# Kernel tuning notes

Hardware: AMD Instinct MI355X
Metric: run time of the kernel (lower is better)

The kernel has to match this reference:

```python
import jax, jax.numpy as jnp
import numpy as np
from jax import lax

B, N, C = 8, 8192, 64
NPOINT, NSAMPLE, RADIUS = 2048, 32, 0.2
EPS = 1e-5


def setup_inputs() -> dict:
    key = jax.random.key(0)
    ks = jax.random.split(key, 14)
    xyz = jax.random.uniform(ks[0], (B, 3, N), dtype=jnp.float32)
    points = jax.random.normal(ks[1], (B, C, N), dtype=jnp.float32)
    dims = [(67, 64), (64, 64), (64, 128)]
    inp = {"xyz": xyz, "points": points}
    for i, (cin, cout) in enumerate(dims, start=1):
        inp[f"W{i}"] = jax.random.normal(ks[2 * i], (cout, cin), dtype=jnp.float32) / np.sqrt(cin)
        inp[f"b{i}"] = jnp.zeros((cout,), jnp.float32)
        inp[f"g{i}"] = jnp.ones((cout,), jnp.float32)
        inp[f"be{i}"] = jnp.zeros((cout,), jnp.float32)
    return inp


def farthest_point_sample(x, npoint):
    # x: [B, N, 3] -> [B, npoint] int32 indices
    b, n, _ = x.shape
    barange = jnp.arange(b)

    def step(carry, _):
        dist, far = carry
        centroid = x[barange, far]                      # [B, 3]
        d = jnp.sum((x - centroid[:, None, :]) ** 2, -1)  # [B, N]
        dist = jnp.minimum(dist, d)
        return (dist, jnp.argmax(dist, -1)), far

    init = (jnp.full((b, n), 1e10, x.dtype), jnp.zeros((b,), jnp.int32))
    _, cents = lax.scan(step, init, None, length=npoint)
    return cents.T  # [B, npoint]


def square_distance(src, dst):
    # src: [B, S, 3], dst: [B, D, 3] -> [B, S, D]
    d = -2.0 * jnp.einsum('bsc,bdc->bsd', src, dst)
    d += jnp.sum(src ** 2, -1)[:, :, None]
    d += jnp.sum(dst ** 2, -1)[:, None, :]
    return d


def query_ball_point(radius, nsample, x, new_x):
    b, n, _ = x.shape
    sqr = square_distance(new_x, x)                    # [B, NP, N]
    idx = jnp.where(sqr > radius ** 2, n, jnp.arange(n)[None, None, :])
    idx = jnp.sort(idx, axis=-1)[:, :, :nsample]       # [B, NP, NS]
    first = idx[:, :, :1]
    return jnp.where(idx == n, first, idx)


def _bn_relu(x, g, be):
    # x: [B, NP, NS, Cout]; batchnorm over (B, NP, NS) per channel (training stats)
    m = x.mean((0, 1, 2))
    v = x.var((0, 1, 2))
    return jax.nn.relu((x - m) * lax.rsqrt(v + EPS) * g + be)


def reference(xyz, points, W1, b1, g1, be1, W2, b2, g2, be2, W3, b3, g3, be3):
    x = xyz.transpose(0, 2, 1)       # [B, N, 3]
    p = points.transpose(0, 2, 1)    # [B, N, C]
    bidx = jnp.arange(B)[:, None, None]

    fps_idx = farthest_point_sample(x, NPOINT)               # [B, NP]
    new_xyz = jnp.take_along_axis(x, fps_idx[:, :, None], 1)  # [B, NP, 3]
    idx = query_ball_point(RADIUS, NSAMPLE, x, new_xyz)       # [B, NP, NS]

    grouped_xyz = x[bidx, idx]                                # [B, NP, NS, 3]
    grouped_norm = grouped_xyz - new_xyz[:, :, None, :]
    grouped_p = p[bidx, idx]                                  # [B, NP, NS, C]
    feat = jnp.concatenate([grouped_norm, grouped_p], -1)     # [B, NP, NS, 3+C]

    for W, b, g, be in ((W1, b1, g1, be1), (W2, b2, g2, be2), (W3, b3, g3, be3)):
        feat = _bn_relu(jnp.einsum('bpsc,oc->bpso', feat, W) + b, g, be)

    new_points = jnp.max(feat, axis=2)                        # [B, NP, Cout]
    return new_xyz.transpose(0, 2, 1), new_points.transpose(0, 2, 1)
```

## Files before the change

### kernel.cpp

```cpp
#include <hip/hip_runtime.h>
#include <hip/hip_bf16.h>
#include <stdint.h>

#define NB 8
#define NPTS 8192
#define NCH 64
#define NPOINT 2048
#define NSAMPLE 32
#define R2 0.04f

#define DPP_MAX_STEP(C) { \
  int lo2_ = __builtin_amdgcn_update_dpp(0, (int)(unsigned int)key, (C), 0xf, 0xf, true); \
  int hi2_ = __builtin_amdgcn_update_dpp(0, (int)(unsigned int)(key>>32), (C), 0xf, 0xf, true); \
  unsigned long long k2_ = ((unsigned long long)(unsigned int)hi2_ << 32) | (unsigned int)lo2_; \
  if (k2_ > key) key = k2_; }

__global__ __launch_bounds__(512) void fps_kernel(const float* __restrict__ xyz,
                                                  float* __restrict__ out)
{
  const int t = threadIdx.x;
  const int wv = t >> 6, lane = t & 63;
  const int b = blockIdx.x;
  const float* xb = xyz + (size_t)b*3*NPTS;
  __shared__ float s_px[NPTS], s_py[NPTS], s_pz[NPTS];
  __shared__ float s_ox[NPOINT], s_oy[NPOINT], s_oz[NPOINT];
  __shared__ unsigned long long s_key[2][8];
  for (int e=t; e<NPTS; e+=512){
    s_px[e]=xb[e]; s_py[e]=xb[NPTS+e]; s_pz[e]=xb[2*NPTS+e];
  }
  float px[16], py[16], pz[16], dist[16];
  const int base = (wv<<10) + lane;
  #pragma unroll
  for (int k=0;k<16;k++){
    int i = base + (k<<6);
    px[k]=xb[i]; py[k]=xb[NPTS+i]; pz[k]=xb[2*NPTS+i];
    dist[k]=1e10f;
  }
  __syncthreads();
  float cx = s_px[0], cy = s_py[0], cz = s_pz[0];
  for (int s=0;s<NPOINT;s++){
    if (t==0){ s_ox[s]=cx; s_oy[s]=cy; s_oz[s]=cz; }
    float best = -1.0f; int bidx = 0;
    #pragma unroll
    for (int k=0;k<16;k++){
      float dx=__fsub_rn(px[k],cx), dy=__fsub_rn(py[k],cy), dz=__fsub_rn(pz[k],cz);
      float d = __fadd_rn(__fadd_rn(__fmul_rn(dx,dx),__fmul_rn(dy,dy)),__fmul_rn(dz,dz));
      float nd = d < dist[k] ? d : dist[k];
      dist[k]=nd;
      if (nd > best){ best = nd; bidx = base + (k<<6); }
    }
    unsigned long long key = ((unsigned long long)__float_as_uint(best) << 13)
                           | (unsigned long long)(8191 - bidx);
    DPP_MAX_STEP(0x111)
    DPP_MAX_STEP(0x112)
    DPP_MAX_STEP(0x114)
    DPP_MAX_STEP(0x118)
    DPP_MAX_STEP(0x142)
    DPP_MAX_STEP(0x143)
    if (lane==63) s_key[s&1][wv] = key;
    __syncthreads();
    const unsigned long long* kr = s_key[s&1];
    unsigned long long k0=kr[0],k1=kr[1],k2=kr[2],k3=kr[3],
                       k4=kr[4],k5=kr[5],k6=kr[6],k7=kr[7];
    unsigned long long m01=k0>k1?k0:k1, m23=k2>k3?k2:k3;
    unsigned long long m45=k4>k5?k4:k5, m67=k6>k7?k6:k7;
    unsigned long long m03=m01>m23?m01:m23, m47=m45>m67?m45:m67;
    unsigned long long mk = m03>m47?m03:m47;
    const int far = 8191 - (int)(mk & 8191ull);
    cx = s_px[far]; cy = s_py[far]; cz = s_pz[far];
  }
  __syncthreads();
  float* oxb = out + (size_t)b*3*NPOINT;
  for (int e=t; e<NPOINT; e+=512){
    oxb[e]          = s_ox[e];
    oxb[NPOINT+e]   = s_oy[e];
    oxb[2*NPOINT+e] = s_oz[e];
  }
}

__global__ __launch_bounds__(256) void ball_kernel(const float* __restrict__ xyz,
                                                   const float* __restrict__ nxyz,
                                                   int* __restrict__ ball_idx)
{
  __shared__ int s_buf[4][NSAMPLE];
  const int wv = threadIdx.x >> 6, lane = threadIdx.x & 63;
  const int g = blockIdx.x*4 + wv;
  const int b = g >> 11;
  const int s = g & 2047;
  const float* ob = nxyz + (size_t)b*3*NPOINT;
  const float cx = ob[s], cy = ob[NPOINT+s], cz = ob[2*NPOINT+s];
  const float csum = __fadd_rn(__fadd_rn(__fmul_rn(cx,cx),__fmul_rn(cy,cy)),__fmul_rn(cz,cz));
  const float* xb = xyz + (size_t)b*3*NPTS;
  int cnt = 0;
  for (int c0=0; c0<NPTS; c0+=64){
    const int i = c0 + lane;
    float x=xb[i], y=xb[NPTS+i], z=xb[2*NPTS+i];
    float dot  = __fmaf_rn(cz, z, __fmaf_rn(cy, y, __fmul_rn(cx, x)));
    float dsum = __fadd_rn(__fadd_rn(__fmul_rn(x,x),__fmul_rn(y,y)),__fmul_rn(z,z));
    float sqr  = __fadd_rn(__fadd_rn(__fmul_rn(-2.0f,dot), csum), dsum);
    bool in = (sqr <= R2);
    unsigned long long m = __ballot(in);
    int rank = cnt + __popcll(m & ((1ull<<lane)-1ull));
    if (in && rank < NSAMPLE) s_buf[wv][rank] = i;
    cnt += (int)__popcll(m);
    if (cnt >= NSAMPLE) break;
  }
  const int first = s_buf[wv][0];
  if (lane < NSAMPLE){
    int v = (lane < cnt) ? s_buf[wv][lane] : first;
    ball_idx[(size_t)g*NSAMPLE + lane] = v;
  }
}

__global__ __launch_bounds__(128) void mlp1_kernel(
    const float* __restrict__ xyz, const float* __restrict__ points,
    const float* __restrict__ nxyz, const int* __restrict__ ball_idx,
    const float* __restrict__ W1, const float* __restrict__ b1,
    float* __restrict__ z, float* __restrict__ part)
{
  __shared__ float wl[67*64];
  __shared__ float spA[128], spQ[128];
  const int t = threadIdx.x;
  const int m = blockIdx.x*128 + t;
  const int g = m >> 5;
  const int b = g >> 11;
  const int s = g & 2047;
  for (int e=t; e<67*64; e+=128){
    int o = e/67, c = e - o*67;
    wl[c*64+o] = W1[e];
  }
  const int idx = ball_idx[m];
  const float* xb = xyz + (size_t)b*3*NPTS;
  const float* ob = nxyz + (size_t)b*3*NPOINT;
  float f[67];
  f[0] = __fsub_rn(xb[idx],        ob[s]);
  f[1] = __fsub_rn(xb[NPTS+idx],   ob[NPOINT+s]);
  f[2] = __fsub_rn(xb[2*NPTS+idx], ob[2*NPOINT+s]);
  const float* pb = points + (size_t)b*NCH*NPTS;
  #pragma unroll
  for (int c=0;c<64;c++) f[3+c] = pb[(size_t)c*NPTS + idx];
  __syncthreads();
  float acc[64];
  #pragma unroll
  for (int o=0;o<64;o++) acc[o]=0.0f;
  #pragma unroll
  for (int c=0;c<67;c++){
    const float fc = f[c];
    const float* wr = &wl[c*64];
    #pragma unroll
    for (int q=0;q<16;q++){
      float4 w = *(const float4*)(wr + q*4);
      acc[q*4+0] = __fmaf_rn(fc, w.x, acc[q*4+0]);
      acc[q*4+1] = __fmaf_rn(fc, w.y, acc[q*4+1]);
      acc[q*4+2] = __fmaf_rn(fc, w.z, acc[q*4+2]);
      acc[q*4+3] = __fmaf_rn(fc, w.w, acc[q*4+3]);
    }
  }
  #pragma unroll
  for (int o=0;o<64;o++) acc[o] = __fadd_rn(acc[o], b1[o]);
  float* zr = z + (size_t)m*64;
  #pragma unroll
  for (int q=0;q<16;q++){
    float4 v; v.x=acc[q*4]; v.y=acc[q*4+1]; v.z=acc[q*4+2]; v.w=acc[q*4+3];
    *(float4*)(zr + q*4) = v;
  }
  float sA=0.f, sQ=0.f;
  const int oc = t & 63;
  for (int p=0;p<2;p++){
    __syncthreads();
    if ((t>>6)==p){
      const int r = t & 63;
      #pragma unroll
      for (int j=0;j<64;j++) wl[r*65+j] = acc[j];
    }
    __syncthreads();
    const int r0 = (t>>6)*32;
    for (int r=r0; r<r0+32; r++){
      float v = wl[r*65+oc];
      sA += v; sQ = __fmaf_rn(v,v,sQ);
    }
  }
  spA[t]=sA; spQ[t]=sQ;
  __syncthreads();
  if (t<64){
    part[(size_t)blockIdx.x*128 + t]      = spA[t]+spA[t+64];
    part[(size_t)blockIdx.x*128 + 64 + t] = spQ[t]+spQ[t+64];
  }
}

__global__ __launch_bounds__(128) void mlp2_kernel(
    float* __restrict__ z, const float* __restrict__ ab1,
    const float* __restrict__ W2, const float* __restrict__ b2,
    float* __restrict__ part)
{
  __shared__ float wl[67*64];
  __shared__ float spA[128], spQ[128];
  __shared__ float s_ab[128];
  const int t = threadIdx.x;
  const int m = blockIdx.x*128 + t;
  for (int e=t; e<64*64; e+=128){
    int o = e>>6, c = e&63;
    wl[c*64+o] = W2[e];
  }
  if (t<128) s_ab[t] = ab1[t];
  __syncthreads();
  float* zr = z + (size_t)m*64;
  float f[64];
  #pragma unroll
  for (int q=0;q<16;q++){
    float4 v = *(const float4*)(zr + q*4);
    float a0 = __fmaf_rn(v.x, s_ab[q*4+0], s_ab[64+q*4+0]);
    float a1 = __fmaf_rn(v.y, s_ab[q*4+1], s_ab[64+q*4+1]);
    float a2 = __fmaf_rn(v.z, s_ab[q*4+2], s_ab[64+q*4+2]);
    float a3 = __fmaf_rn(v.w, s_ab[q*4+3], s_ab[64+q*4+3]);
    f[q*4+0] = a0 > 0.f ? a0 : 0.f;
    f[q*4+1] = a1 > 0.f ? a1 : 0.f;
    f[q*4+2] = a2 > 0.f ? a2 : 0.f;
    f[q*4+3] = a3 > 0.f ? a3 : 0.f;
  }
  float acc[64];
  #pragma unroll
  for (int o=0;o<64;o++) acc[o]=0.0f;
  #pragma unroll
  for (int c=0;c<64;c++){
    const float fc = f[c];
    const float* wr = &wl[c*64];
    #pragma unroll
    for (int q=0;q<16;q++){
      float4 w = *(const float4*)(wr + q*4);
      acc[q*4+0] = __fmaf_rn(fc, w.x, acc[q*4+0]);
      acc[q*4+1] = __fmaf_rn(fc, w.y, acc[q*4+1]);
      acc[q*4+2] = __fmaf_rn(fc, w.z, acc[q*4+2]);
      acc[q*4+3] = __fmaf_rn(fc, w.w, acc[q*4+3]);
    }
  }
  #pragma unroll
  for (int o=0;o<64;o++) acc[o] = __fadd_rn(acc[o], b2[o]);
  #pragma unroll
  for (int q=0;q<16;q++){
    float4 v; v.x=acc[q*4]; v.y=acc[q*4+1]; v.z=acc[q*4+2]; v.w=acc[q*4+3];
    *(float4*)(zr + q*4) = v;
  }
  float sA=0.f, sQ=0.f;
  const int oc = t & 63;
  for (int p=0;p<2;p++){
    __syncthreads();
    if ((t>>6)==p){
      const int r = t & 63;
      #pragma unroll
      for (int j=0;j<64;j++) wl[r*65+j] = acc[j];
    }
    __syncthreads();
    const int r0 = (t>>6)*32;
    for (int r=r0; r<r0+32; r++){
      float v = wl[r*65+oc];
      sA += v; sQ = __fmaf_rn(v,v,sQ);
    }
  }
  spA[t]=sA; spQ[t]=sQ;
  __syncthreads();
  if (t<64){
    part[(size_t)blockIdx.x*128 + t]      = spA[t]+spA[t+64];
    part[(size_t)blockIdx.x*128 + 64 + t] = spQ[t]+spQ[t+64];
  }
}

__global__ __launch_bounds__(256) void mlp3_kernel(
    const float* __restrict__ z, const float* __restrict__ ab2,
    const float* __restrict__ W3, const float* __restrict__ b3,
    float* __restrict__ gmax, float* __restrict__ part)
{
  __shared__ float wl[128*65];
  __shared__ float spA[256], spQ[256];
  __shared__ float s_ab[128];
  const int t = threadIdx.x;
  const int m0 = blockIdx.x*128;
  const int sm = t>>1, h = t&1;
  const int m = m0 + sm;
  for (int e=t; e<64*128; e+=256){
    int o = e>>6, c = e&63;
    wl[c*128+o] = W3[e];
  }
  if (t<128) s_ab[t] = ab2[t];
  __syncthreads();
  const float* zr = z + (size_t)m*64;
  float f[64];
  #pragma unroll
  for (int q=0;q<16;q++){
    float4 v = *(const float4*)(zr + q*4);
    float a0 = __fmaf_rn(v.x, s_ab[q*4+0], s_ab[64+q*4+0]);
    float a1 = __fmaf_rn(v.y, s_ab[q*4+1], s_ab[64+q*4+1]);
    float a2 = __fmaf_rn(v.z, s_ab[q*4+2], s_ab[64+q*4+2]);
    float a3 = __fmaf_rn(v.w, s_ab[q*4+3], s_ab[64+q*4+3]);
    f[q*4+0] = a0 > 0.f ? a0 : 0.f;
    f[q*4+1] = a1 > 0.f ? a1 : 0.f;
    f[q*4+2] = a2 > 0.f ? a2 : 0.f;
    f[q*4+3] = a3 > 0.f ? a3 : 0.f;
  }
  float acc[64];
  #pragma unroll
  for (int o=0;o<64;o++) acc[o]=0.0f;
  #pragma unroll
  for (int c=0;c<64;c++){
    const float fc = f[c];
    const float* wr = &wl[c*128 + h*64];
    #pragma unroll
    for (int q=0;q<16;q++){
      float4 w = *(const float4*)(wr + q*4);
      acc[q*4+0] = __fmaf_rn(fc, w.x, acc[q*4+0]);
      acc[q*4+1] = __fmaf_rn(fc, w.y, acc[q*4+1]);
      acc[q*4+2] = __fmaf_rn(fc, w.z, acc[q*4+2]);
      acc[q*4+3] = __fmaf_rn(fc, w.w, acc[q*4+3]);
    }
  }
  #pragma unroll
  for (int j=0;j<64;j++) acc[j] = __fadd_rn(acc[j], b3[h*64+j]);
  for (int p=0;p<2;p++){
    __syncthreads();
    if (h==p){
      const int r = sm;
      #pragma unroll
      for (int j=0;j<64;j++) wl[r*65+j] = acc[j];
    }
    __syncthreads();
    const int oc = t & 63;
    const int q4 = t >> 6;
    float sA=0.f, sQ=0.f;
    for (int r=q4*32; r<q4*32+32; r++){
      float v = wl[r*65+oc];
      sA += v; sQ = __fmaf_rn(v,v,sQ);
    }
    spA[t]=sA; spQ[t]=sQ;
    __syncthreads();
    if (t<64){
      float A = spA[t]+spA[t+64]+spA[t+128]+spA[t+192];
      float Q = spQ[t]+spQ[t+64]+spQ[t+128]+spQ[t+192];
      part[(size_t)blockIdx.x*256 + p*64 + t]       = A;
      part[(size_t)blockIdx.x*256 + 128 + p*64 + t] = Q;
    }
  }
  #pragma unroll
  for (int off=2; off<64; off<<=1){
    #pragma unroll
    for (int j=0;j<64;j++){
      float ov = __shfl_xor(acc[j], off, 64);
      acc[j] = acc[j] > ov ? acc[j] : ov;
    }
  }
  const int lane = t & 63, w = t >> 6;
  const int gg = (m0>>5) + w;
  if (lane < 2){
    float* gp = gmax + (size_t)gg*128 + lane*64;
    #pragma unroll
    for (int q=0;q<16;q++){
      float4 v; v.x=acc[q*4]; v.y=acc[q*4+1]; v.z=acc[q*4+2]; v.w=acc[q*4+3];
      *(float4*)(gp + q*4) = v;
    }
  }
}

__global__ __launch_bounds__(64) void reduce_kernel(const float* __restrict__ part,
    const float* __restrict__ gw, const float* __restrict__ bew,
    float* __restrict__ ab, int cout, int nblk)
{
  const int o = blockIdx.x, t = threadIdx.x;
  const int stride = 2*cout;
  float A=0.f, Q=0.f;
  for (int i=t;i<nblk;i+=64){
    A += part[(size_t)i*stride + o];
    Q += part[(size_t)i*stride + cout + o];
  }
  #pragma unroll
  for (int off=1; off<64; off<<=1){
    A += __shfl_xor(A, off, 64);
    Q += __shfl_xor(Q, off, 64);
  }
  if (t==0){
    const float inv = 1.0f/524288.0f;
    float mean = A*inv;
    float var  = Q*inv - mean*mean;
    float a = gw[o] / sqrtf(var + 1e-5f);
    ab[o] = a;
    ab[cout+o] = bew[o] - mean*a;
  }
}

__global__ __launch_bounds__(256) void final_kernel(const float* __restrict__ gmax,
    const float* __restrict__ ab3, float* __restrict__ out)
{
  __shared__ float tile[32*129];
  __shared__ float s_a[128], s_b[128];
  const int t = threadIdx.x;
  const int b = blockIdx.x >> 6;
  const int s0 = (blockIdx.x & 63)*32;
  if (t<128){ s_a[t]=ab3[t]; s_b[t]=ab3[128+t]; }
  const float* gp = gmax + ((size_t)b*NPOINT + s0)*128;
  for (int e=t; e<32*32; e+=256){
    int r = e>>5, q = e&31;
    float4 v = *(const float4*)(gp + r*128 + q*4);
    tile[r*129 + q*4+0]=v.x; tile[r*129 + q*4+1]=v.y;
    tile[r*129 + q*4+2]=v.z; tile[r*129 + q*4+3]=v.w;
  }
  __syncthreads();
  float* ob = out + 49152 + (size_t)b*128*NPOINT;
  for (int e=t; e<128*32; e+=256){
    int o = e>>5, ls = e&31;
    float v = tile[ls*129 + o];
    v = __fmaf_rn(v, s_a[o], s_b[o]);
    v = v > 0.f ? v : 0.f;
    ob[(size_t)o*NPOINT + s0 + ls] = v;
  }
}

extern "C" void kernel_launch(void* const* d_in, const int* in_sizes, int n_in,
                              void* d_out, int out_size, void* d_ws, size_t ws_size,
                              hipStream_t stream)
{
  const float* xyz    = (const float*)d_in[0];
  const float* points = (const float*)d_in[1];
  const float* W1 = (const float*)d_in[2];
  const float* b1 = (const float*)d_in[3];
  const float* g1 = (const float*)d_in[4];
  const float* be1= (const float*)d_in[5];
  const float* W2 = (const float*)d_in[6];
  const float* b2 = (const float*)d_in[7];
  const float* g2 = (const float*)d_in[8];
  const float* be2= (const float*)d_in[9];
  const float* W3 = (const float*)d_in[10];
  const float* b3 = (const float*)d_in[11];
  const float* g3 = (const float*)d_in[12];
  const float* be3= (const float*)d_in[13];
  float* out = (float*)d_out;
  char* ws = (char*)d_ws;
  float* z     = (float*)(ws);
  float* gmax  = (float*)(ws + 134217728);
  int*   ball  = (int*)  (ws + 142606336);
  float* part1 = (float*)(ws + 144703488);
  float* part2 = (float*)(ws + 146800640);
  float* part3 = (float*)(ws + 148897792);
  float* ab1   = (float*)(ws + 153092096);
  float* ab2   = (float*)(ws + 153092608);
  float* ab3   = (float*)(ws + 153093120);

  hipLaunchKernelGGL(fps_kernel,   dim3(NB),   dim3(512),  0, stream, xyz, out);
  hipLaunchKernelGGL(ball_kernel,  dim3(4096), dim3(256),  0, stream, xyz, out, ball);
  hipLaunchKernelGGL(mlp1_kernel,  dim3(4096), dim3(128),  0, stream, xyz, points, out, ball, W1, b1, z, part1);
  hipLaunchKernelGGL(reduce_kernel,dim3(64),   dim3(64),   0, stream, part1, g1, be1, ab1, 64, 4096);
  hipLaunchKernelGGL(mlp2_kernel,  dim3(4096), dim3(128),  0, stream, z, ab1, W2, b2, part2);
  hipLaunchKernelGGL(reduce_kernel,dim3(64),   dim3(64),   0, stream, part2, g2, be2, ab2, 64, 4096);
  hipLaunchKernelGGL(mlp3_kernel,  dim3(4096), dim3(256),  0, stream, z, ab2, W3, b3, gmax, part3);
  hipLaunchKernelGGL(reduce_kernel,dim3(128),  dim3(64),   0, stream, part3, g3, be3, ab3, 128, 4096);
  hipLaunchKernelGGL(final_kernel, dim3(512),  dim3(256),  0, stream, gmax, ab3, out);
}
```

Baseline: 2.683 ms.

## Fuse ball query into MLP1, pre-transpose points, store activations channel-major

Adds a transpose kernel so each gathered neighbour's 64 features form one contiguous row read with float4 loads, replacing 64 strided scalar gathers. The ball query is merged into the first MLP kernel, which removes the ball_idx round trip through global memory and one launch. The intermediate z buffer becomes channel-major per block, so per-thread accesses in mlp1/2/3 coalesce across threads. The cost is an extra transpose pass over the point features and a ball-query stage that now uses only two waves per block, run serially for four centroids.

```diff
diff --git a/kernel.cpp b/kernel.cpp
--- a/kernel.cpp
+++ b/kernel.cpp
@@ -78,68 +78,89 @@
   }
 }
 
-__global__ __launch_bounds__(256) void ball_kernel(const float* __restrict__ xyz,
-                                                   const float* __restrict__ nxyz,
-                                                   int* __restrict__ ball_idx)
-{
-  __shared__ int s_buf[4][NSAMPLE];
-  const int wv = threadIdx.x >> 6, lane = threadIdx.x & 63;
-  const int g = blockIdx.x*4 + wv;
-  const int b = g >> 11;
-  const int s = g & 2047;
-  const float* ob = nxyz + (size_t)b*3*NPOINT;
-  const float cx = ob[s], cy = ob[NPOINT+s], cz = ob[2*NPOINT+s];
-  const float csum = __fadd_rn(__fadd_rn(__fmul_rn(cx,cx),__fmul_rn(cy,cy)),__fmul_rn(cz,cz));
-  const float* xb = xyz + (size_t)b*3*NPTS;
-  int cnt = 0;
-  for (int c0=0; c0<NPTS; c0+=64){
-    const int i = c0 + lane;
-    float x=xb[i], y=xb[NPTS+i], z=xb[2*NPTS+i];
-    float dot  = __fmaf_rn(cz, z, __fmaf_rn(cy, y, __fmul_rn(cx, x)));
-    float dsum = __fadd_rn(__fadd_rn(__fmul_rn(x,x),__fmul_rn(y,y)),__fmul_rn(z,z));
-    float sqr  = __fadd_rn(__fadd_rn(__fmul_rn(-2.0f,dot), csum), dsum);
-    bool in = (sqr <= R2);
-    unsigned long long m = __ballot(in);
-    int rank = cnt + __popcll(m & ((1ull<<lane)-1ull));
-    if (in && rank < NSAMPLE) s_buf[wv][rank] = i;
-    cnt += (int)__popcll(m);
-    if (cnt >= NSAMPLE) break;
-  }
-  const int first = s_buf[wv][0];
-  if (lane < NSAMPLE){
-    int v = (lane < cnt) ? s_buf[wv][lane] : first;
-    ball_idx[(size_t)g*NSAMPLE + lane] = v;
-  }
-}
-
-__global__ __launch_bounds__(128) void mlp1_kernel(
-    const float* __restrict__ xyz, const float* __restrict__ points,
-    const float* __restrict__ nxyz, const int* __restrict__ ball_idx,
+__global__ __launch_bounds__(256) void transpose_kernel(const float* __restrict__ points,
+                                                        float* __restrict__ pt)
+{
+  __shared__ float tile[64][65];
+  const int t = threadIdx.x;
+  const int b  = blockIdx.x >> 7;
+  const int n0 = (blockIdx.x & 127) << 6;
+  const int tx = t & 63, ty = t >> 6;
+  #pragma unroll
+  for (int r=0; r<16; r++){
+    const int c = ty*16 + r;
+    tile[c][tx] = points[(size_t)b*NCH*NPTS + (size_t)c*NPTS + n0 + tx];
+  }
+  __syncthreads();
+  #pragma unroll
+  for (int r=0; r<16; r++){
+    const int n = ty*16 + r;
+    pt[((size_t)b*NPTS + n0 + n)*64 + tx] = tile[tx][n];
+  }
+}
+
+__global__ __launch_bounds__(128) void ballmlp1_kernel(
+    const float* __restrict__ xyz, const float* __restrict__ pt,
+    const float* __restrict__ nxyz,
     const float* __restrict__ W1, const float* __restrict__ b1,
     float* __restrict__ z, float* __restrict__ part)
 {
   __shared__ float wl[67*64];
   __shared__ float spA[128], spQ[128];
-  const int t = threadIdx.x;
-  const int m = blockIdx.x*128 + t;
-  const int g = m >> 5;
-  const int b = g >> 11;
-  const int s = g & 2047;
+  __shared__ int s_buf[4][NSAMPLE];
+  __shared__ int s_cnt[4];
+  __shared__ float s_ctr[4][3];
+  const int t = threadIdx.x;
+  const int blk = blockIdx.x;
   for (int e=t; e<67*64; e+=128){
     int o = e/67, c = e - o*67;
     wl[c*64+o] = W1[e];
   }
-  const int idx = ball_idx[m];
+  const int wv = t>>6, lane = t&63;
+  for (int sub=0; sub<2; sub++){
+    const int gi2 = wv*2 + sub;
+    const int g = blk*4 + gi2;
+    const int b = g >> 11;
+    const int s = g & 2047;
+    const float* ob = nxyz + (size_t)b*3*NPOINT;
+    const float cx = ob[s], cy = ob[NPOINT+s], cz = ob[2*NPOINT+s];
+    if (lane==0){ s_ctr[gi2][0]=cx; s_ctr[gi2][1]=cy; s_ctr[gi2][2]=cz; }
+    const float csum = __fadd_rn(__fadd_rn(__fmul_rn(cx,cx),__fmul_rn(cy,cy)),__fmul_rn(cz,cz));
+    const float* xb = xyz + (size_t)b*3*NPTS;
+    int cnt = 0;
+    for (int c0=0; c0<NPTS; c0+=64){
+      const int i = c0 + lane;
+      float x=xb[i], y=xb[NPTS+i], zz=xb[2*NPTS+i];
+      float dot  = __fmaf_rn(cz, zz, __fmaf_rn(cy, y, __fmul_rn(cx, x)));
+      float dsum = __fadd_rn(__fadd_rn(__fmul_rn(x,x),__fmul_rn(y,y)),__fmul_rn(zz,zz));
+      float sqr  = __fadd_rn(__fadd_rn(__fmul_rn(-2.0f,dot), csum), dsum);
+      bool in = (sqr <= R2);
+      unsigned long long mm = __ballot(in);
+      int rank = cnt + __popcll(mm & ((1ull<<lane)-1ull));
+      if (in && rank < NSAMPLE) s_buf[gi2][rank] = i;
+      cnt += (int)__popcll(mm);
+      if (cnt >= NSAMPLE) break;
+    }
+    if (lane==0) s_cnt[gi2] = cnt;
+  }
+  __syncthreads();
+  const int gi = t>>5, lane2 = t&31;
+  const int g = blk*4 + gi;
+  const int b = g >> 11;
+  const int cnt = s_cnt[gi];
+  const int first = s_buf[gi][0];
+  const int idx = (lane2 < cnt) ? s_buf[gi][lane2] : first;
   const float* xb = xyz + (size_t)b*3*NPTS;
-  const float* ob = nxyz + (size_t)b*3*NPOINT;
   float f[67];
-  f[0] = __fsub_rn(xb[idx],        ob[s]);
-  f[1] = __fsub_rn(xb[NPTS+idx],   ob[NPOINT+s]);
-  f[2] = __fsub_rn(xb[2*NPTS+idx], ob[2*NPOINT+s]);
-  const float* pb = points + (size_t)b*NCH*NPTS;
-  #pragma unroll
-  for (int c=0;c<64;c++) f[3+c] = pb[(size_t)c*NPTS + idx];
-  __syncthreads();
+  f[0] = __fsub_rn(xb[idx],        s_ctr[gi][0]);
+  f[1] = __fsub_rn(xb[NPTS+idx],   s_ctr[gi][1]);
+  f[2] = __fsub_rn(xb[2*NPTS+idx], s_ctr[gi][2]);
+  const float* pr = pt + ((size_t)b*NPTS + idx)*64;
+  #pragma unroll
+  for (int q=0;q<16;q++){
+    float4 v = *(const float4*)(pr + q*4);
+    f[3+q*4+0]=v.x; f[3+q*4+1]=v.y; f[3+q*4+2]=v.z; f[3+q*4+3]=v.w;
+  }
   float acc[64];
   #pragma unroll
   for (int o=0;o<64;o++) acc[o]=0.0f;
@@ -158,12 +179,9 @@
   }
   #pragma unroll
   for (int o=0;o<64;o++) acc[o] = __fadd_rn(acc[o], b1[o]);
-  float* zr = z + (size_t)m*64;
-  #pragma unroll
-  for (int q=0;q<16;q++){
-    float4 v; v.x=acc[q*4]; v.y=acc[q*4+1]; v.z=acc[q*4+2]; v.w=acc[q*4+3];
-    *(float4*)(zr + q*4) = v;
-  }
+  float* zb = z + (size_t)blk*8192;
+  #pragma unroll
+  for (int c=0;c<64;c++) zb[c*128 + t] = acc[c];
   float sA=0.f, sQ=0.f;
   const int oc = t & 63;
   for (int p=0;p<2;p++){
@@ -183,8 +201,8 @@
   spA[t]=sA; spQ[t]=sQ;
   __syncthreads();
   if (t<64){
-    part[(size_t)blockIdx.x*128 + t]      = spA[t]+spA[t+64];
-    part[(size_t)blockIdx.x*128 + 64 + t] = spQ[t]+spQ[t+64];
+    part[(size_t)blk*128 + t]      = spA[t]+spA[t+64];
+    part[(size_t)blk*128 + 64 + t] = spQ[t]+spQ[t+64];
   }
 }
 
@@ -197,26 +215,19 @@
   __shared__ float spA[128], spQ[128];
   __shared__ float s_ab[128];
   const int t = threadIdx.x;
-  const int m = blockIdx.x*128 + t;
   for (int e=t; e<64*64; e+=128){
     int o = e>>6, c = e&63;
     wl[c*64+o] = W2[e];
   }
   if (t<128) s_ab[t] = ab1[t];
   __syncthreads();
-  float* zr = z + (size_t)m*64;
+  float* zb = z + (size_t)blockIdx.x*8192;
   float f[64];
   #pragma unroll
-  for (int q=0;q<16;q++){
-    float4 v = *(const float4*)(zr + q*4);
-    float a0 = __fmaf_rn(v.x, s_ab[q*4+0], s_ab[64+q*4+0]);
-    float a1 = __fmaf_rn(v.y, s_ab[q*4+1], s_ab[64+q*4+1]);
-    float a2 = __fmaf_rn(v.z, s_ab[q*4+2], s_ab[64+q*4+2]);
-    float a3 = __fmaf_rn(v.w, s_ab[q*4+3], s_ab[64+q*4+3]);
-    f[q*4+0] = a0 > 0.f ? a0 : 0.f;
-    f[q*4+1] = a1 > 0.f ? a1 : 0.f;
-    f[q*4+2] = a2 > 0.f ? a2 : 0.f;
-    f[q*4+3] = a3 > 0.f ? a3 : 0.f;
+  for (int c=0;c<64;c++){
+    float v = zb[c*128 + t];
+    float a = __fmaf_rn(v, s_ab[c], s_ab[64+c]);
+    f[c] = a > 0.f ? a : 0.f;
   }
   float acc[64];
   #pragma unroll
@@ -237,10 +248,7 @@
   #pragma unroll
   for (int o=0;o<64;o++) acc[o] = __fadd_rn(acc[o], b2[o]);
   #pragma unroll
-  for (int q=0;q<16;q++){
-    float4 v; v.x=acc[q*4]; v.y=acc[q*4+1]; v.z=acc[q*4+2]; v.w=acc[q*4+3];
-    *(float4*)(zr + q*4) = v;
-  }
+  for (int c=0;c<64;c++) zb[c*128 + t] = acc[c];
   float sA=0.f, sQ=0.f;
   const int oc = t & 63;
   for (int p=0;p<2;p++){
@@ -276,26 +284,19 @@
   const int t = threadIdx.x;
   const int m0 = blockIdx.x*128;
   const int sm = t>>1, h = t&1;
-  const int m = m0 + sm;
   for (int e=t; e<64*128; e+=256){
     int o = e>>6, c = e&63;
     wl[c*128+o] = W3[e];
   }
   if (t<128) s_ab[t] = ab2[t];
   __syncthreads();
-  const float* zr = z + (size_t)m*64;
+  const float* zb = z + (size_t)blockIdx.x*8192;
   float f[64];
   #pragma unroll
-  for (int q=0;q<16;q++){
-    float4 v = *(const float4*)(zr + q*4);
-    float a0 = __fmaf_rn(v.x, s_ab[q*4+0], s_ab[64+q*4+0]);
-    float a1 = __fmaf_rn(v.y, s_ab[q*4+1], s_ab[64+q*4+1]);
-    float a2 = __fmaf_rn(v.z, s_ab[q*4+2], s_ab[64+q*4+2]);
-    float a3 = __fmaf_rn(v.w, s_ab[q*4+3], s_ab[64+q*4+3]);
-    f[q*4+0] = a0 > 0.f ? a0 : 0.f;
-    f[q*4+1] = a1 > 0.f ? a1 : 0.f;
-    f[q*4+2] = a2 > 0.f ? a2 : 0.f;
-    f[q*4+3] = a3 > 0.f ? a3 : 0.f;
+  for (int c=0;c<64;c++){
+    float v = zb[c*128 + sm];
+    float a = __fmaf_rn(v, s_ab[c], s_ab[64+c]);
+    f[c] = a > 0.f ? a : 0.f;
   }
   float acc[64];
   #pragma unroll
@@ -433,22 +434,22 @@
   float* out = (float*)d_out;
   char* ws = (char*)d_ws;
   float* z     = (float*)(ws);
+  float* pt    = (float*)(ws + 134217728);
   float* gmax  = (float*)(ws + 134217728);
-  int*   ball  = (int*)  (ws + 142606336);
-  float* part1 = (float*)(ws + 144703488);
+  float* part3 = (float*)(ws + 142606336);
   float* part2 = (float*)(ws + 146800640);
-  float* part3 = (float*)(ws + 148897792);
+  float* part1 = (float*)(ws + 150994944);
   float* ab1   = (float*)(ws + 153092096);
   float* ab2   = (float*)(ws + 153092608);
   float* ab3   = (float*)(ws + 153093120);
 
-  hipLaunchKernelGGL(fps_kernel,   dim3(NB),   dim3(512),  0, stream, xyz, out);
-  hipLaunchKernelGGL(ball_kernel,  dim3(4096), dim3(256),  0, stream, xyz, out, ball);
-  hipLaunchKernelGGL(mlp1_kernel,  dim3(4096), dim3(128),  0, stream, xyz, points, out, ball, W1, b1, z, part1);
-  hipLaunchKernelGGL(reduce_kernel,dim3(64),   dim3(64),   0, stream, part1, g1, be1, ab1, 64, 4096);
-  hipLaunchKernelGGL(mlp2_kernel,  dim3(4096), dim3(128),  0, stream, z, ab1, W2, b2, part2);
-  hipLaunchKernelGGL(reduce_kernel,dim3(64),   dim3(64),   0, stream, part2, g2, be2, ab2, 64, 4096);
-  hipLaunchKernelGGL(mlp3_kernel,  dim3(4096), dim3(256),  0, stream, z, ab2, W3, b3, gmax, part3);
-  hipLaunchKernelGGL(reduce_kernel,dim3(128),  dim3(64),   0, stream, part3, g3, be3, ab3, 128, 4096);
-  hipLaunchKernelGGL(final_kernel, dim3(512),  dim3(256),  0, stream, gmax, ab3, out);
-}
+  hipLaunchKernelGGL(fps_kernel,      dim3(NB),   dim3(512), 0, stream, xyz, out);
+  hipLaunchKernelGGL(transpose_kernel,dim3(1024), dim3(256), 0, stream, points, pt);
+  hipLaunchKernelGGL(ballmlp1_kernel, dim3(4096), dim3(128), 0, stream, xyz, pt, out, W1, b1, z, part1);
+  hipLaunchKernelGGL(reduce_kernel,   dim3(64),   dim3(64),  0, stream, part1, g1, be1, ab1, 64, 4096);
+  hipLaunchKernelGGL(mlp2_kernel,     dim3(4096), dim3(128), 0, stream, z, ab1, W2, b2, part2);
+  hipLaunchKernelGGL(reduce_kernel,   dim3(64),   dim3(64),  0, stream, part2, g2, be2, ab2, 64, 4096);
+  hipLaunchKernelGGL(mlp3_kernel,     dim3(4096), dim3(256), 0, stream, z, ab2, W3, b3, gmax, part3);
+  hipLaunchKernelGGL(reduce_kernel,   dim3(128),  dim3(64),  0, stream, part3, g3, be3, ab3, 128, 4096);
+  hipLaunchKernelGGL(final_kernel,    dim3(512),  dim3(256), 0, stream, gmax, ab3, out);
+}
```

New measurement: 2.575 ms. 4.1% less time.
